# Kernel optimization log

Hardware: AMD Instinct MI355X
Metric: run time of the kernel (lower is better)

The kernel has to match this reference:

```python
import jax, jax.numpy as jnp
import numpy as np
from jax import lax

STEPS = 4
MULT = 4
N_MIX = 14  # sum(2+i for i in range(STEPS))
BN_SCALE = float(1.0 / np.sqrt(1.0 + 1e-5))  # eval-mode BatchNorm, affine=False, default running stats (mean=0, var=1)


def _bn(x):
    return x * jnp.asarray(BN_SCALE, x.dtype)


def _conv1x1(x, w):  # x [B,Ci,H,W], w [Co,Ci]
    return jnp.einsum('bihw,oi->bohw', x, w)


def _dwconv(x, w, pad, dil=1):  # depthwise conv, w [C,k,k]
    C = w.shape[0]
    return lax.conv_general_dilated(x, w[:, None], (1, 1),
                                    [(pad, pad), (pad, pad)],
                                    rhs_dilation=(dil, dil),
                                    dimension_numbers=('NCHW', 'OIHW', 'NCHW'),
                                    feature_group_count=C)


def _maxpool3(x):
    return lax.reduce_window(x, -jnp.inf, lax.max, (1, 1, 3, 3), (1, 1, 1, 1),
                             [(0, 0), (0, 0), (1, 1), (1, 1)])


def _avgpool3(x):  # count_include_pad=False as in torch avg_pool2d used by DARTS
    s = lax.reduce_window(x, 0.0, lax.add, (1, 1, 3, 3), (1, 1, 1, 1),
                          [(0, 0), (0, 0), (1, 1), (1, 1)])
    ones = jnp.ones(x.shape[2:], x.dtype)
    cnt = lax.reduce_window(ones, 0.0, lax.add, (3, 3), (1, 1), [(1, 1), (1, 1)])
    return s / cnt


def _sep_conv(x, dw1, pw1, dw2, pw2, pad):
    y = _bn(_conv1x1(_dwconv(jax.nn.relu(x), dw1, pad), pw1))
    return _bn(_conv1x1(_dwconv(jax.nn.relu(y), dw2, pad), pw2))


def _dil_conv(x, dw, pw, pad):
    return _bn(_conv1x1(_dwconv(jax.nn.relu(x), dw, pad, dil=2), pw))


def setup_inputs():
    key = jax.random.key(0)
    B, C_in, C, H, W = 32, 512, 128, 32, 32
    ks = jax.random.split(key, 24)
    rn = lambda k, shp, s=0.05: jax.random.normal(k, shp, jnp.float32) * s
    return {
        's0': jax.random.normal(ks[0], (B, C_in, H, W), jnp.float32),
        's1': jax.random.normal(ks[1], (B, C_in, H, W), jnp.float32),
        'gates': jax.random.normal(ks[2], (N_MIX, B, 8), jnp.float32),
        'pre0_w': rn(ks[3], (C, C_in)),
        'pre1_w': rn(ks[4], (C, C_in)),
        'sep3_dw1': rn(ks[5], (N_MIX, C, 3, 3), 0.2),
        'sep3_pw1': rn(ks[6], (N_MIX, C, C)),
        'sep3_dw2': rn(ks[7], (N_MIX, C, 3, 3), 0.2),
        'sep3_pw2': rn(ks[8], (N_MIX, C, C)),
        'sep5_dw1': rn(ks[9], (N_MIX, C, 5, 5), 0.2),
        'sep5_pw1': rn(ks[10], (N_MIX, C, C)),
        'sep5_dw2': rn(ks[11], (N_MIX, C, 5, 5), 0.2),
        'sep5_pw2': rn(ks[12], (N_MIX, C, C)),
        'dil3_dw': rn(ks[13], (N_MIX, C, 3, 3), 0.2),
        'dil3_pw': rn(ks[14], (N_MIX, C, C)),
        'dil5_dw': rn(ks[15], (N_MIX, C, 5, 5), 0.2),
        'dil5_pw': rn(ks[16], (N_MIX, C, C)),
        'top': 2,
    }


def reference(s0, s1, gates, pre0_w, pre1_w,
              sep3_dw1, sep3_pw1, sep3_dw2, sep3_pw2,
              sep5_dw1, sep5_pw1, sep5_dw2, sep5_pw2,
              dil3_dw, dil3_pw, dil5_dw, dil5_pw, top):
    def mixed(x, gate, m):
        # MixedOp.forward with external weights (is_first=False): top-k mask,
        # masked softmax -> per-sample alphas that are exactly 0 off the top-k,
        # weighted sum over candidate ops (dense form of the scatter-add dispatch).
        B = gate.shape[0]
        _, idx = lax.top_k(gate, top)  # [B, top]
        mask = jnp.zeros(gate.shape, bool).at[jnp.arange(B)[:, None], idx].set(True)
        p = jax.nn.softmax(jnp.where(mask, gate, -jnp.inf), axis=-1)  # [B, 8]
        w = lambda o: p[:, o][:, None, None, None]
        # PRIMITIVES order: none, max_pool_3x3, avg_pool_3x3, skip_connect,
        #                   sep_conv_3x3, sep_conv_5x5, dil_conv_3x3, dil_conv_5x5
        out = w(1) * _bn(_maxpool3(x)) + w(2) * _bn(_avgpool3(x)) + w(3) * x
        out = out + w(4) * _sep_conv(x, sep3_dw1[m], sep3_pw1[m], sep3_dw2[m], sep3_pw2[m], 1)
        out = out + w(5) * _sep_conv(x, sep5_dw1[m], sep5_pw1[m], sep5_dw2[m], sep5_pw2[m], 2)
        out = out + w(6) * _dil_conv(x, dil3_dw[m], dil3_pw[m], 2)
        out = out + w(7) * _dil_conv(x, dil5_dw[m], dil5_pw[m], 4)
        return out

    # preprocess0/1: ReLUConvBN 1x1 (reduction_prev=False)
    s0 = _bn(_conv1x1(jax.nn.relu(s0), pre0_w))
    s1 = _bn(_conv1x1(jax.nn.relu(s1), pre1_w))
    states = [s0, s1]
    offset = 0
    for i in range(STEPS):
        s = sum(mixed(h, gates[offset + j], offset + j) for j, h in enumerate(states))
        offset += len(states)
        states.append(s)
    return jnp.concatenate(states[-MULT:], axis=1)  # [B, MULT*C, H, W]
```

## Files before the change

### kernel.cpp

```cpp
#include <hip/hip_runtime.h>

#define BN_S 0.9999950000374997f

typedef __attribute__((ext_vector_type(8))) short bf16x8;
typedef __attribute__((ext_vector_type(4))) float f32x4;

__device__ inline short f2bf(float f) {
    union { float f; unsigned u; } v; v.f = f;
    return (short)((v.u + 0x7FFFu + ((v.u >> 16) & 1u)) >> 16);
}

__global__ void gates_k(const float* __restrict__ g, const int* __restrict__ topp,
                        float* __restrict__ p)
{
    int t = blockIdx.x * blockDim.x + threadIdx.x;
    if (t >= 14 * 32) return;
    int top = topp[0];
    float v[8]; bool sel[8];
    for (int o = 0; o < 8; ++o) { v[o] = g[t * 8 + o]; sel[o] = false; }
    for (int it = 0; it < top; ++it) {
        int bi = 0; float bv = -3.4e38f;
        for (int o = 0; o < 8; ++o)
            if (!sel[o] && v[o] > bv) { bv = v[o]; bi = o; }
        sel[bi] = true;
    }
    float mx = -3.4e38f;
    for (int o = 0; o < 8; ++o) if (sel[o]) mx = fmaxf(mx, v[o]);
    float e[8]; float sum = 0.0f;
    for (int o = 0; o < 8; ++o) { e[o] = sel[o] ? expf(v[o] - mx) : 0.0f; sum += e[o]; }
    for (int o = 0; o < 8; ++o) p[t * 8 + o] = e[o] / sum;
}

__global__ void cvt_k(const float* __restrict__ s3p1, const float* __restrict__ s3p2,
                      const float* __restrict__ s5p1, const float* __restrict__ s5p2,
                      const float* __restrict__ d3p,  const float* __restrict__ d5p,
                      const float* __restrict__ pre0, const float* __restrict__ pre1,
                      short* __restrict__ wb, short* __restrict__ wpre)
{
    const int which = blockIdx.y;
    const float* src; short* dst; int n;
    switch (which) {
        case 0: src = s3p1; dst = wb;               n = 229376; break;
        case 1: src = s3p2; dst = wb + 229376;      n = 229376; break;
        case 2: src = s5p1; dst = wb + 2 * 229376;  n = 229376; break;
        case 3: src = s5p2; dst = wb + 3 * 229376;  n = 229376; break;
        case 4: src = d3p;  dst = wb + 4 * 229376;  n = 229376; break;
        case 5: src = d5p;  dst = wb + 5 * 229376;  n = 229376; break;
        case 6: src = pre0; dst = wpre;             n = 65536;  break;
        default:src = pre1; dst = wpre + 65536;     n = 65536;  break;
    }
    for (int i = blockIdx.x * 256 + threadIdx.x; i < n; i += gridDim.x * 256)
        dst[i] = f2bf(src[i]);
}

__global__ void __launch_bounds__(256)
pre_k(const float* __restrict__ s0, const float* __restrict__ s1,
      const short* __restrict__ wpre,
      float* __restrict__ s0p, float* __restrict__ s1p)
{
    const int z = blockIdx.z;
    const int b = z & 31, which = z >> 5;
    const float* in = (which ? s1 : s0) + (long)b * 524288;
    const short* w = wpre + which * 65536;
    float* outp = (which ? s1p : s0p) + (long)b * 131072;

    const int tid = threadIdx.x;
    const int wave = tid >> 6, lane = tid & 63;
    const int quad = lane >> 4, l16 = lane & 15;
    const int n0 = blockIdx.x * 128;

    __shared__ short bt[128 * 40];
    const int tn = tid & 127, tk = (tid >> 7) * 16;

    f32x4 acc[16];
#pragma unroll
    for (int i = 0; i < 16; ++i) acc[i] = (f32x4){0.f, 0.f, 0.f, 0.f};

    for (int k0 = 0; k0 < 512; k0 += 32) {
        __syncthreads();
        bf16x8 lo, hi;
#pragma unroll
        for (int kk = 0; kk < 8; ++kk) {
            lo[kk] = f2bf(fmaxf(in[(long)(k0 + tk + kk) * 1024 + n0 + tn], 0.0f));
            hi[kk] = f2bf(fmaxf(in[(long)(k0 + tk + 8 + kk) * 1024 + n0 + tn], 0.0f));
        }
        *(bf16x8*)&bt[tn * 40 + tk]     = lo;
        *(bf16x8*)&bt[tn * 40 + tk + 8] = hi;
        __syncthreads();
#pragma unroll
        for (int cf = 0; cf < 2; ++cf) {
            bf16x8 af = *(const bf16x8*)(w + (long)(wave * 32 + cf * 16 + l16) * 512
                                           + k0 + quad * 8);
#pragma unroll
            for (int s = 0; s < 8; ++s) {
                bf16x8 bfv = *(const bf16x8*)&bt[(s * 16 + l16) * 40 + quad * 8];
                acc[cf * 8 + s] = __builtin_amdgcn_mfma_f32_16x16x32_bf16(
                                      af, bfv, acc[cf * 8 + s], 0, 0, 0);
            }
        }
    }
#pragma unroll
    for (int cf = 0; cf < 2; ++cf)
#pragma unroll
        for (int s = 0; s < 8; ++s)
#pragma unroll
            for (int r = 0; r < 4; ++r)
                outp[(long)(wave * 32 + cf * 16 + quad * 4 + r) * 1024
                     + n0 + s * 16 + l16] = acc[cf * 8 + s][r] * BN_S;
}

template<int KS, int DIL, int PAD>
__device__ inline float dwc(const float* t, const float* w, int h, int wx) {
    float s = 0.0f;
#pragma unroll
    for (int ki = 0; ki < KS; ++ki) {
        int y = h - PAD + ki * DIL;
        if ((unsigned)y < 32u) {
#pragma unroll
            for (int kj = 0; kj < KS; ++kj) {
                int x = wx - PAD + kj * DIL;
                if ((unsigned)x < 32u) s += w[ki * KS + kj] * t[(y << 5) + x];
            }
        }
    }
    return s;
}

struct BranchA {
    const float* xs[5]; long xbs[5];
    int goff[5]; int m[5]; int nb;
};


__global__ void __launch_bounds__(256)
dw1_all(BranchA a, const float* __restrict__ s3d1, const float* __restrict__ s5d1,
        const float* __restrict__ d3d, const float* __restrict__ d5d,
        short* __restrict__ X, const float* __restrict__ p)
{
    const int c = blockIdx.x, b = blockIdx.y, j = blockIdx.z;
    const float* pm = p + a.goff[j] + b * 8;
    const float g4 = pm[4], g5 = pm[5], g6 = pm[6], g7 = pm[7];
    if (g4 == 0.f && g5 == 0.f && g6 == 0.f && g7 == 0.f) return;
    const int m = a.m[j];
    __shared__ float t[1024];
    __shared__ float wl[4][25];
    const int tid = threadIdx.x;
    const float* src = a.xs[j] + (long)b * a.xbs[j] + (long)c * 1024;
    for (int i = tid; i < 1024; i += 256) t[i] = fmaxf(src[i], 0.0f);
    if (tid < 9)                      wl[0][tid]     = s3d1[(long)m * 1152 + (long)c * 9 + tid];
    else if (tid >= 64 && tid < 89)   wl[1][tid-64]  = s5d1[(long)m * 3200 + (long)c * 25 + tid - 64];
    else if (tid >= 128 && tid < 137) wl[2][tid-128] = d3d[(long)m * 1152 + (long)c * 9 + tid - 128];
    else if (tid >= 192 && tid < 217) wl[3][tid-192] = d5d[(long)m * 3200 + (long)c * 25 + tid - 192];
    __syncthreads();
    short* dst = X + (long)j * 16777216 + (long)b * 524288 + (long)c * 1024;
    const float s6 = g6 * BN_S, s7 = g7 * BN_S;
    for (int i = tid; i < 1024; i += 256) {
        int h = i >> 5, wx = i & 31;
        if (g4 != 0.f) dst[i]          = f2bf(dwc<3,1,1>(t, wl[0], h, wx));
        if (g5 != 0.f) dst[131072 + i] = f2bf(dwc<5,1,2>(t, wl[1], h, wx));
        if (g6 != 0.f) dst[262144 + i] = f2bf(s6 * dwc<3,2,2>(t, wl[2], h, wx));
        if (g7 != 0.f) dst[393216 + i] = f2bf(s7 * dwc<5,2,4>(t, wl[3], h, wx));
    }
}

__global__ void __launch_bounds__(256)
pw1_all(BranchA a, const short* __restrict__ X, const short* __restrict__ wb,
        float* __restrict__ yb, const float* __restrict__ p)
{
    const int z = blockIdx.z, b = z & 31, j = z >> 5;
    const int u = blockIdx.y >> 2, cot = blockIdx.y & 3;
    if (p[a.goff[j] + b * 8 + 4 + u] == 0.f) return;
    const int tid = threadIdx.x;
    const int wave = tid >> 6, lane = tid & 63;
    const int quad = lane >> 4, l16 = lane & 15;
    const int co0 = cot * 32 + (wave & 1) * 16;
    const int n0  = blockIdx.x * 128 + (wave >> 1) * 64;
    const short* w = wb + (u ? 2L * 229376 : 0L) + (long)a.m[j] * 16384;
    const short* xb = X + (long)j * 16777216 + (long)b * 524288 + (long)u * 131072;

    f32x4 acc[4] = {{0,0,0,0},{0,0,0,0},{0,0,0,0},{0,0,0,0}};
    for (int k0 = 0; k0 < 128; k0 += 32) {
        bf16x8 af = *(const bf16x8*)(w + (co0 + l16) * 128 + k0 + quad * 8);
        const short* xc = xb + (long)(k0 + quad * 8) * 1024 + n0 + l16;
#pragma unroll
        for (int s = 0; s < 4; ++s) {
            bf16x8 bfv;
#pragma unroll
            for (int jj = 0; jj < 8; ++jj) bfv[jj] = xc[jj * 1024 + s * 16];
            acc[s] = __builtin_amdgcn_mfma_f32_16x16x32_bf16(af, bfv, acc[s], 0, 0, 0);
        }
    }
    float* dst = yb + (long)j * 8388608 + ((long)b * 2 + u) * 131072;
#pragma unroll
    for (int s = 0; s < 4; ++s)
#pragma unroll
        for (int r = 0; r < 4; ++r)
            dst[(long)(co0 + quad * 4 + r) * 1024 + n0 + s * 16 + l16] =
                fmaxf(acc[s][r] * BN_S, 0.0f);
}

__global__ void __launch_bounds__(256)
dw2_all(BranchA a, const float* __restrict__ yb,
        const float* __restrict__ s3d2, const float* __restrict__ s5d2,
        short* __restrict__ X, const float* __restrict__ p)
{
    const int c = blockIdx.x, b = blockIdx.y;
    const int z = blockIdx.z, u = z & 1, j = z >> 1;
    const float g = p[a.goff[j] + b * 8 + 4 + u];
    if (g == 0.f) return;
    const int m = a.m[j];
    __shared__ float t[1024];
    __shared__ float wl[25];
    const int tid = threadIdx.x;
    const float* src = yb + (long)j * 8388608 + ((long)b * 2 + u) * 131072 + (long)c * 1024;
    for (int i = tid; i < 1024; i += 256) t[i] = src[i];
    if (u == 0) { if (tid < 9)  wl[tid] = s3d2[(long)m * 1152 + (long)c * 9  + tid]; }
    else        { if (tid < 25) wl[tid] = s5d2[(long)m * 3200 + (long)c * 25 + tid]; }
    __syncthreads();
    const float sc = g * BN_S;
    short* dst = X + (long)j * 16777216 + (long)b * 524288 + (long)u * 131072 + (long)c * 1024;
    if (u == 0) {
        for (int i = tid; i < 1024; i += 256)
            dst[i] = f2bf(sc * dwc<3,1,1>(t, wl, i >> 5, i & 31));
    } else {
        for (int i = tid; i < 1024; i += 256)
            dst[i] = f2bf(sc * dwc<5,1,2>(t, wl, i >> 5, i & 31));
    }
}

__global__ void __launch_bounds__(256)
final_all(BranchA a, const short* __restrict__ X, const short* __restrict__ wb,
          float* __restrict__ outp, const float* __restrict__ p)
{
    const int b = blockIdx.z;
    const int tid = threadIdx.x;
    const int wave = tid >> 6, lane = tid & 63;
    const int quad = lane >> 4, l16 = lane & 15;
    const int co0 = blockIdx.y * 32 + (wave & 1) * 16;
    const int n0  = blockIdx.x * 128 + (wave >> 1) * 64;

    f32x4 acc[4] = {{0,0,0,0},{0,0,0,0},{0,0,0,0},{0,0,0,0}};
    bool any = false;
    for (int j = 0; j < a.nb; ++j) {
        const float* pm = p + a.goff[j] + b * 8;
        const short* xj = X + (long)j * 16777216 + (long)b * 524288;
        const long wm = (long)a.m[j] * 16384;
        const short* ws_[4] = { wb + 1L * 229376 + wm, wb + 3L * 229376 + wm,
                                wb + 4L * 229376 + wm, wb + 5L * 229376 + wm };
#pragma unroll
        for (int seg = 0; seg < 4; ++seg) {
            if (pm[4 + seg] == 0.f) continue;
            any = true;
            const short* w = ws_[seg];
            const short* xs = xj + (long)seg * 131072;
            for (int k0 = 0; k0 < 128; k0 += 32) {
                bf16x8 af = *(const bf16x8*)(w + (co0 + l16) * 128 + k0 + quad * 8);
                const short* xc = xs + (long)(k0 + quad * 8) * 1024 + n0 + l16;
#pragma unroll
                for (int s = 0; s < 4; ++s) {
                    bf16x8 bfv;
#pragma unroll
                    for (int jj = 0; jj < 8; ++jj) bfv[jj] = xc[jj * 1024 + s * 16];
                    acc[s] = __builtin_amdgcn_mfma_f32_16x16x32_bf16(af, bfv, acc[s], 0, 0, 0);
                }
            }
        }
    }
    if (!any) return;
#pragma unroll
    for (int s = 0; s < 4; ++s)
#pragma unroll
        for (int r = 0; r < 4; ++r) {
            long idx = (long)b * 524288 + (long)(co0 + quad * 4 + r) * 1024
                     + n0 + s * 16 + l16;
            outp[idx] += acc[s][r];
        }
}

struct PoolA { const float* xs[5]; long xbs[5]; int goff[5]; int cnt; };

__global__ void __launch_bounds__(256)
pool_skip_all_k(PoolA a, const float* __restrict__ p,
                float* __restrict__ so, long out_bs)
{
    const int c = blockIdx.x, b = blockIdx.y, tid = threadIdx.x;
    __shared__ float t[1024];
    float acc[4] = {0.f, 0.f, 0.f, 0.f};
    for (int j = 0; j < a.cnt; ++j) {
        const float* g = p + a.goff[j] + b * 8;
        float w1 = g[1] * BN_S, w2 = g[2] * BN_S, w3 = g[3];
        if (w1 == 0.f && w2 == 0.f && w3 == 0.f) continue;
        const float* src = a.xs[j] + (long)b * a.xbs[j] + (long)c * 1024;
        __syncthreads();
        for (int i = tid; i < 1024; i += 256) t[i] = src[i];
        __syncthreads();
#pragma unroll
        for (int e = 0; e < 4; ++e) {
            int i = tid + e * 256;
            int h = i >> 5, wx = i & 31;
            int y0 = max(h - 1, 0), y1 = min(h + 1, 31);
            int x0 = max(wx - 1, 0), x1 = min(wx + 1, 31);
            float mx = -3.4e38f, sm = 0.0f;
            for (int y = y0; y <= y1; ++y)
                for (int x = x0; x <= x1; ++x) {
                    float v = t[(y << 5) + x];
                    mx = fmaxf(mx, v); sm += v;
                }
            float cntc = (float)((y1 - y0 + 1) * (x1 - x0 + 1));
            acc[e] += w1 * mx + w2 * (sm / cntc) + w3 * t[i];
        }
    }
    float* dst = so + (long)b * out_bs + (long)c * 1024;
#pragma unroll
    for (int e = 0; e < 4; ++e) dst[tid + e * 256] = acc[e];
}

extern "C" void kernel_launch(void* const* d_in, const int* in_sizes, int n_in,
                              void* d_out, int out_size, void* d_ws, size_t ws_size,
                              hipStream_t stream)
{
    const float* s0   = (const float*)d_in[0];
    const float* s1   = (const float*)d_in[1];
    const float* gts  = (const float*)d_in[2];
    const float* pre0 = (const float*)d_in[3];
    const float* pre1 = (const float*)d_in[4];
    const float* s3d1 = (const float*)d_in[5];
    const float* s3p1 = (const float*)d_in[6];
    const float* s3d2 = (const float*)d_in[7];
    const float* s3p2 = (const float*)d_in[8];
    const float* s5d1 = (const float*)d_in[9];
    const float* s5p1 = (const float*)d_in[10];
    const float* s5d2 = (const float*)d_in[11];
    const float* s5p2 = (const float*)d_in[12];
    const float* d3d  = (const float*)d_in[13];
    const float* d3p  = (const float*)d_in[14];
    const float* d5d  = (const float*)d_in[15];
    const float* d5p  = (const float*)d_in[16];
    const int*   topp = (const int*)d_in[17];
    float* out = (float*)d_out;

    float* ws   = (float*)d_ws;
    float* p    = ws;
    float* s0p  = ws + 4096;
    float* s1p  = s0p + 4194304;
    short* wb   = (short*)(s1p + 4194304);
    short* wpre = wb + 1376256;
    char*  sl   = (char*)(wpre + 131072);
    uintptr_t ua = ((uintptr_t)sl + 255) & ~(uintptr_t)255;
    short* X    = (short*)ua;

    size_t used_base = (size_t)((char*)ua - (char*)d_ws);
    const size_t slot_bytes = 16777216ull * 2 + 8388608ull * 4;
    int nslot = 1;
    if (ws_size > used_base + slot_bytes)
        nslot = (int)((ws_size - used_base) / slot_bytes);
    if (nslot > 5) nslot = 5;
    if (nslot < 1) nslot = 1;
    float* yb = (float*)(X + (long)nslot * 16777216);

    gates_k<<<2, 256, 0, stream>>>(gts, topp, p);
    cvt_k<<<dim3(224, 8), 256, 0, stream>>>(s3p1, s3p2, s5p1, s5p2, d3p, d5p,
                                            pre0, pre1, wb, wpre);
    pre_k<<<dim3(8, 1, 64), 256, 0, stream>>>(s0, s1, wpre, s0p, s1p);

    const long SB = 131072L, OB = 524288L;
    const float* stp[6]; long sbs[6];
    stp[0] = s0p; sbs[0] = SB;
    stp[1] = s1p; sbs[1] = SB;

    int offset = 0;
    for (int i = 0; i < 4; ++i) {
        float* so = out + (long)i * 131072;
        int cnt = 2 + i;

        PoolA pa{};
        for (int j = 0; j < cnt; ++j) {
            pa.xs[j] = stp[j]; pa.xbs[j] = sbs[j]; pa.goff[j] = (offset + j) * 256;
        }
        pa.cnt = cnt;
        pool_skip_all_k<<<dim3(128, 32), 256, 0, stream>>>(pa, p, so, OB);

        for (int j0 = 0; j0 < cnt; j0 += nslot) {
            int nb = (cnt - j0 < nslot) ? (cnt - j0) : nslot;
            BranchA a{};
            for (int jj = 0; jj < nb; ++jj) {
                int j = j0 + jj, m = offset + j;
                a.xs[jj] = stp[j]; a.xbs[jj] = sbs[j];
                a.goff[jj] = m * 256; a.m[jj] = m;
            }
            a.nb = nb;
            dw1_all<<<dim3(128, 32, nb), 256, 0, stream>>>(a, s3d1, s5d1, d3d, d5d, X, p);
            pw1_all<<<dim3(8, 8, 32 * nb), 256, 0, stream>>>(a, X, wb, yb, p);
            dw2_all<<<dim3(128, 32, 2 * nb), 256, 0, stream>>>(a, yb, s3d2, s5d2, X, p);
            final_all<<<dim3(8, 4, 32), 256, 0, stream>>>(a, X, wb, so, p);
        }
        stp[2 + i] = so; sbs[2 + i] = OB;
        offset += cnt;
    }
}
```

Measured before the change: 935.2 us.

## Pad depthwise tiles in LDS, compute 4 outputs per thread, widen pre_k

The depthwise conv kernels now stage a zero-padded halo tile in shared memory, which removes the per-tap bounds checks. Each thread computes four adjacent output pixels and writes them as a single packed 4x bf16 store, so neighbouring taps are reused from registers. The preprocess GEMM kernel moves to 512 threads per block, with each wave handling 16 output channels instead of 32. This raises wave count per tile and halves the accumulator registers per thread, at the cost of more threads sharing each shared-memory tile load.

```diff
diff --git a/kernel.cpp b/kernel.cpp
--- a/kernel.cpp
+++ b/kernel.cpp
@@ -3,6 +3,7 @@
 #define BN_S 0.9999950000374997f
 
 typedef __attribute__((ext_vector_type(8))) short bf16x8;
+typedef __attribute__((ext_vector_type(4))) short s16x4;
 typedef __attribute__((ext_vector_type(4))) float f32x4;
 
 __device__ inline short f2bf(float f) {
@@ -53,7 +54,7 @@
         dst[i] = f2bf(src[i]);
 }
 
-__global__ void __launch_bounds__(256)
+__global__ void __launch_bounds__(512)
 pre_k(const float* __restrict__ s0, const float* __restrict__ s1,
       const short* __restrict__ wpre,
       float* __restrict__ s0p, float* __restrict__ s1p)
@@ -70,60 +71,33 @@
     const int n0 = blockIdx.x * 128;
 
     __shared__ short bt[128 * 40];
-    const int tn = tid & 127, tk = (tid >> 7) * 16;
-
-    f32x4 acc[16];
-#pragma unroll
-    for (int i = 0; i < 16; ++i) acc[i] = (f32x4){0.f, 0.f, 0.f, 0.f};
+    const int tn = tid & 127, tk = (tid >> 7) * 8;
+
+    f32x4 acc[8];
+#pragma unroll
+    for (int i = 0; i < 8; ++i) acc[i] = (f32x4){0.f, 0.f, 0.f, 0.f};
 
     for (int k0 = 0; k0 < 512; k0 += 32) {
         __syncthreads();
-        bf16x8 lo, hi;
-#pragma unroll
-        for (int kk = 0; kk < 8; ++kk) {
-            lo[kk] = f2bf(fmaxf(in[(long)(k0 + tk + kk) * 1024 + n0 + tn], 0.0f));
-            hi[kk] = f2bf(fmaxf(in[(long)(k0 + tk + 8 + kk) * 1024 + n0 + tn], 0.0f));
-        }
-        *(bf16x8*)&bt[tn * 40 + tk]     = lo;
-        *(bf16x8*)&bt[tn * 40 + tk + 8] = hi;
+        bf16x8 v;
+#pragma unroll
+        for (int kk = 0; kk < 8; ++kk)
+            v[kk] = f2bf(fmaxf(in[(long)(k0 + tk + kk) * 1024 + n0 + tn], 0.0f));
+        *(bf16x8*)&bt[tn * 40 + tk] = v;
         __syncthreads();
-#pragma unroll
-        for (int cf = 0; cf < 2; ++cf) {
-            bf16x8 af = *(const bf16x8*)(w + (long)(wave * 32 + cf * 16 + l16) * 512
-                                           + k0 + quad * 8);
-#pragma unroll
-            for (int s = 0; s < 8; ++s) {
-                bf16x8 bfv = *(const bf16x8*)&bt[(s * 16 + l16) * 40 + quad * 8];
-                acc[cf * 8 + s] = __builtin_amdgcn_mfma_f32_16x16x32_bf16(
-                                      af, bfv, acc[cf * 8 + s], 0, 0, 0);
-            }
-        }
-    }
-#pragma unroll
-    for (int cf = 0; cf < 2; ++cf)
-#pragma unroll
-        for (int s = 0; s < 8; ++s)
-#pragma unroll
-            for (int r = 0; r < 4; ++r)
-                outp[(long)(wave * 32 + cf * 16 + quad * 4 + r) * 1024
-                     + n0 + s * 16 + l16] = acc[cf * 8 + s][r] * BN_S;
-}
-
-template<int KS, int DIL, int PAD>
-__device__ inline float dwc(const float* t, const float* w, int h, int wx) {
-    float s = 0.0f;
-#pragma unroll
-    for (int ki = 0; ki < KS; ++ki) {
-        int y = h - PAD + ki * DIL;
-        if ((unsigned)y < 32u) {
-#pragma unroll
-            for (int kj = 0; kj < KS; ++kj) {
-                int x = wx - PAD + kj * DIL;
-                if ((unsigned)x < 32u) s += w[ki * KS + kj] * t[(y << 5) + x];
-            }
-        }
-    }
-    return s;
+        bf16x8 af = *(const bf16x8*)(w + (long)(wave * 16 + l16) * 512 + k0 + quad * 8);
+#pragma unroll
+        for (int s = 0; s < 8; ++s) {
+            bf16x8 bfv = *(const bf16x8*)&bt[(s * 16 + l16) * 40 + quad * 8];
+            acc[s] = __builtin_amdgcn_mfma_f32_16x16x32_bf16(af, bfv, acc[s], 0, 0, 0);
+        }
+    }
+#pragma unroll
+    for (int s = 0; s < 8; ++s)
+#pragma unroll
+        for (int r = 0; r < 4; ++r)
+            outp[(long)(wave * 16 + quad * 4 + r) * 1024 + n0 + s * 16 + l16] =
+                acc[s][r] * BN_S;
 }
 
 struct BranchA {
@@ -142,24 +116,86 @@
     const float g4 = pm[4], g5 = pm[5], g6 = pm[6], g7 = pm[7];
     if (g4 == 0.f && g5 == 0.f && g6 == 0.f && g7 == 0.f) return;
     const int m = a.m[j];
-    __shared__ float t[1024];
+    __shared__ float t[40 * 40];
     __shared__ float wl[4][25];
     const int tid = threadIdx.x;
     const float* src = a.xs[j] + (long)b * a.xbs[j] + (long)c * 1024;
-    for (int i = tid; i < 1024; i += 256) t[i] = fmaxf(src[i], 0.0f);
+    for (int i = tid; i < 1600; i += 256) {
+        int r = i / 40, col = i - r * 40;
+        int y = r - 4, x = col - 4;
+        float v = 0.0f;
+        if ((unsigned)y < 32u && (unsigned)x < 32u) v = fmaxf(src[(y << 5) + x], 0.0f);
+        t[i] = v;
+    }
     if (tid < 9)                      wl[0][tid]     = s3d1[(long)m * 1152 + (long)c * 9 + tid];
     else if (tid >= 64 && tid < 89)   wl[1][tid-64]  = s5d1[(long)m * 3200 + (long)c * 25 + tid - 64];
     else if (tid >= 128 && tid < 137) wl[2][tid-128] = d3d[(long)m * 1152 + (long)c * 9 + tid - 128];
     else if (tid >= 192 && tid < 217) wl[3][tid-192] = d5d[(long)m * 3200 + (long)c * 25 + tid - 192];
     __syncthreads();
     short* dst = X + (long)j * 16777216 + (long)b * 524288 + (long)c * 1024;
+    const int h = tid >> 3, w0 = (tid & 7) * 4;
+    const float* tc = &t[(h + 4) * 40 + (w0 + 4)];
     const float s6 = g6 * BN_S, s7 = g7 * BN_S;
-    for (int i = tid; i < 1024; i += 256) {
-        int h = i >> 5, wx = i & 31;
-        if (g4 != 0.f) dst[i]          = f2bf(dwc<3,1,1>(t, wl[0], h, wx));
-        if (g5 != 0.f) dst[131072 + i] = f2bf(dwc<5,1,2>(t, wl[1], h, wx));
-        if (g6 != 0.f) dst[262144 + i] = f2bf(s6 * dwc<3,2,2>(t, wl[2], h, wx));
-        if (g7 != 0.f) dst[393216 + i] = f2bf(s7 * dwc<5,2,4>(t, wl[3], h, wx));
+
+    if (g4 != 0.f) {
+        float a0 = 0.f, a1 = 0.f, a2 = 0.f, a3 = 0.f;
+#pragma unroll
+        for (int ki = 0; ki < 3; ++ki) {
+            const float* row = tc + (ki - 1) * 40;
+#pragma unroll
+            for (int kj = 0; kj < 3; ++kj) {
+                float wv = wl[0][ki * 3 + kj];
+                a0 += wv * row[kj - 1]; a1 += wv * row[kj];
+                a2 += wv * row[kj + 1]; a3 += wv * row[kj + 2];
+            }
+        }
+        *(s16x4*)&dst[tid * 4] = (s16x4){f2bf(a0), f2bf(a1), f2bf(a2), f2bf(a3)};
+    }
+    if (g5 != 0.f) {
+        float a0 = 0.f, a1 = 0.f, a2 = 0.f, a3 = 0.f;
+#pragma unroll
+        for (int ki = 0; ki < 5; ++ki) {
+            const float* row = tc + (ki - 2) * 40;
+#pragma unroll
+            for (int kj = 0; kj < 5; ++kj) {
+                float wv = wl[1][ki * 5 + kj];
+                a0 += wv * row[kj - 2]; a1 += wv * row[kj - 1];
+                a2 += wv * row[kj];     a3 += wv * row[kj + 1];
+            }
+        }
+        *(s16x4*)&dst[131072 + tid * 4] = (s16x4){f2bf(a0), f2bf(a1), f2bf(a2), f2bf(a3)};
+    }
+    if (g6 != 0.f) {
+        float a0 = 0.f, a1 = 0.f, a2 = 0.f, a3 = 0.f;
+#pragma unroll
+        for (int ki = 0; ki < 3; ++ki) {
+            const float* row = tc + (ki * 2 - 2) * 40;
+#pragma unroll
+            for (int kj = 0; kj < 3; ++kj) {
+                float wv = wl[2][ki * 3 + kj];
+                int o = kj * 2 - 2;
+                a0 += wv * row[o];     a1 += wv * row[o + 1];
+                a2 += wv * row[o + 2]; a3 += wv * row[o + 3];
+            }
+        }
+        *(s16x4*)&dst[262144 + tid * 4] =
+            (s16x4){f2bf(s6 * a0), f2bf(s6 * a1), f2bf(s6 * a2), f2bf(s6 * a3)};
+    }
+    if (g7 != 0.f) {
+        float a0 = 0.f, a1 = 0.f, a2 = 0.f, a3 = 0.f;
+#pragma unroll
+        for (int ki = 0; ki < 5; ++ki) {
+            const float* row = tc + (ki * 2 - 4) * 40;
+#pragma unroll
+            for (int kj = 0; kj < 5; ++kj) {
+                float wv = wl[3][ki * 5 + kj];
+                int o = kj * 2 - 4;
+                a0 += wv * row[o];     a1 += wv * row[o + 1];
+                a2 += wv * row[o + 2]; a3 += wv * row[o + 3];
+            }
+        }
+        *(s16x4*)&dst[393216 + tid * 4] =
+            (s16x4){f2bf(s7 * a0), f2bf(s7 * a1), f2bf(s7 * a2), f2bf(s7 * a3)};
     }
 }
 
@@ -209,23 +245,50 @@
     const float g = p[a.goff[j] + b * 8 + 4 + u];
     if (g == 0.f) return;
     const int m = a.m[j];
-    __shared__ float t[1024];
+    __shared__ float t[36 * 36];
     __shared__ float wl[25];
     const int tid = threadIdx.x;
     const float* src = yb + (long)j * 8388608 + ((long)b * 2 + u) * 131072 + (long)c * 1024;
-    for (int i = tid; i < 1024; i += 256) t[i] = src[i];
+    for (int i = tid; i < 1296; i += 256) {
+        int r = i / 36, col = i - r * 36;
+        int y = r - 2, x = col - 2;
+        float v = 0.0f;
+        if ((unsigned)y < 32u && (unsigned)x < 32u) v = src[(y << 5) + x];
+        t[i] = v;
+    }
     if (u == 0) { if (tid < 9)  wl[tid] = s3d2[(long)m * 1152 + (long)c * 9  + tid]; }
     else        { if (tid < 25) wl[tid] = s5d2[(long)m * 3200 + (long)c * 25 + tid]; }
     __syncthreads();
     const float sc = g * BN_S;
     short* dst = X + (long)j * 16777216 + (long)b * 524288 + (long)u * 131072 + (long)c * 1024;
+    const int h = tid >> 3, w0 = (tid & 7) * 4;
+    const float* tc = &t[(h + 2) * 36 + (w0 + 2)];
+    float a0 = 0.f, a1 = 0.f, a2 = 0.f, a3 = 0.f;
     if (u == 0) {
-        for (int i = tid; i < 1024; i += 256)
-            dst[i] = f2bf(sc * dwc<3,1,1>(t, wl, i >> 5, i & 31));
+#pragma unroll
+        for (int ki = 0; ki < 3; ++ki) {
+            const float* row = tc + (ki - 1) * 36;
+#pragma unroll
+            for (int kj = 0; kj < 3; ++kj) {
+                float wv = wl[ki * 3 + kj];
+                a0 += wv * row[kj - 1]; a1 += wv * row[kj];
+                a2 += wv * row[kj + 1]; a3 += wv * row[kj + 2];
+            }
+        }
     } else {
-        for (int i = tid; i < 1024; i += 256)
-            dst[i] = f2bf(sc * dwc<5,1,2>(t, wl, i >> 5, i & 31));
-    }
+#pragma unroll
+        for (int ki = 0; ki < 5; ++ki) {
+            const float* row = tc + (ki - 2) * 36;
+#pragma unroll
+            for (int kj = 0; kj < 5; ++kj) {
+                float wv = wl[ki * 5 + kj];
+                a0 += wv * row[kj - 2]; a1 += wv * row[kj - 1];
+                a2 += wv * row[kj];     a3 += wv * row[kj + 1];
+            }
+        }
+    }
+    *(s16x4*)&dst[tid * 4] =
+        (s16x4){f2bf(sc * a0), f2bf(sc * a1), f2bf(sc * a2), f2bf(sc * a3)};
 }
 
 __global__ void __launch_bounds__(256)
@@ -361,7 +424,7 @@
     gates_k<<<2, 256, 0, stream>>>(gts, topp, p);
     cvt_k<<<dim3(224, 8), 256, 0, stream>>>(s3p1, s3p2, s5p1, s5p2, d3p, d5p,
                                             pre0, pre1, wb, wpre);
-    pre_k<<<dim3(8, 1, 64), 256, 0, stream>>>(s0, s1, wpre, s0p, s1p);
+    pre_k<<<dim3(8, 1, 64), 512, 0, stream>>>(s0, s1, wpre, s0p, s1p);
 
     const long SB = 131072L, OB = 524288L;
     const float* stp[6]; long sbs[6];
```

Result: faster. 814.7 us (-12.9%).

## Store depthwise outputs channel-interleaved and register-prefetch preprocess GEMM

Applied to the files above, without the earlier changes.

The depthwise kernels now process groups of 8 channels per block from a zero-padded shared tile. They write bf16 outputs in a [channel-group][pixel][8] interleaved layout, so the pointwise MFMA kernels can load each B fragment with one 16-byte vector load instead of eight strided scalar loads. The preprocess GEMM is retiled to 64 columns with 512 threads and prefetches the next K slice into registers to overlap global loads with MFMA. The cost is more shared memory per depthwise block (about 51KB) and fewer depthwise blocks, which may reduce occupancy.

```diff
diff --git a/kernel.cpp b/kernel.cpp
--- a/kernel.cpp
+++ b/kernel.cpp
@@ -3,6 +3,7 @@
 #define BN_S 0.9999950000374997f
 
 typedef __attribute__((ext_vector_type(8))) short bf16x8;
+typedef __attribute__((ext_vector_type(4))) short s16x4;
 typedef __attribute__((ext_vector_type(4))) float f32x4;
 
 __device__ inline short f2bf(float f) {
@@ -53,7 +54,7 @@
         dst[i] = f2bf(src[i]);
 }
 
-__global__ void __launch_bounds__(256)
+__global__ void __launch_bounds__(512)
 pre_k(const float* __restrict__ s0, const float* __restrict__ s1,
       const short* __restrict__ wpre,
       float* __restrict__ s0p, float* __restrict__ s1p)
@@ -67,63 +68,45 @@
     const int tid = threadIdx.x;
     const int wave = tid >> 6, lane = tid & 63;
     const int quad = lane >> 4, l16 = lane & 15;
-    const int n0 = blockIdx.x * 128;
-
-    __shared__ short bt[128 * 40];
-    const int tn = tid & 127, tk = (tid >> 7) * 16;
-
-    f32x4 acc[16];
-#pragma unroll
-    for (int i = 0; i < 16; ++i) acc[i] = (f32x4){0.f, 0.f, 0.f, 0.f};
+    const int n0 = blockIdx.x * 64;
+
+    __shared__ short bt[64 * 40];
+    const int tn = tid & 63, tk4 = (tid >> 6) * 4;
+
+    float r[4];
+#pragma unroll
+    for (int kk = 0; kk < 4; ++kk)
+        r[kk] = in[(long)(tk4 + kk) * 1024 + n0 + tn];
+
+    f32x4 acc[4];
+#pragma unroll
+    for (int i = 0; i < 4; ++i) acc[i] = (f32x4){0.f, 0.f, 0.f, 0.f};
 
     for (int k0 = 0; k0 < 512; k0 += 32) {
         __syncthreads();
-        bf16x8 lo, hi;
-#pragma unroll
-        for (int kk = 0; kk < 8; ++kk) {
-            lo[kk] = f2bf(fmaxf(in[(long)(k0 + tk + kk) * 1024 + n0 + tn], 0.0f));
-            hi[kk] = f2bf(fmaxf(in[(long)(k0 + tk + 8 + kk) * 1024 + n0 + tn], 0.0f));
-        }
-        *(bf16x8*)&bt[tn * 40 + tk]     = lo;
-        *(bf16x8*)&bt[tn * 40 + tk + 8] = hi;
+        s16x4 v;
+#pragma unroll
+        for (int kk = 0; kk < 4; ++kk) v[kk] = f2bf(fmaxf(r[kk], 0.0f));
+        *(s16x4*)&bt[tn * 40 + tk4] = v;
         __syncthreads();
-#pragma unroll
-        for (int cf = 0; cf < 2; ++cf) {
-            bf16x8 af = *(const bf16x8*)(w + (long)(wave * 32 + cf * 16 + l16) * 512
-                                           + k0 + quad * 8);
-#pragma unroll
-            for (int s = 0; s < 8; ++s) {
-                bf16x8 bfv = *(const bf16x8*)&bt[(s * 16 + l16) * 40 + quad * 8];
-                acc[cf * 8 + s] = __builtin_amdgcn_mfma_f32_16x16x32_bf16(
-                                      af, bfv, acc[cf * 8 + s], 0, 0, 0);
-            }
-        }
-    }
-#pragma unroll
-    for (int cf = 0; cf < 2; ++cf)
-#pragma unroll
-        for (int s = 0; s < 8; ++s)
-#pragma unroll
-            for (int r = 0; r < 4; ++r)
-                outp[(long)(wave * 32 + cf * 16 + quad * 4 + r) * 1024
-                     + n0 + s * 16 + l16] = acc[cf * 8 + s][r] * BN_S;
-}
-
-template<int KS, int DIL, int PAD>
-__device__ inline float dwc(const float* t, const float* w, int h, int wx) {
-    float s = 0.0f;
-#pragma unroll
-    for (int ki = 0; ki < KS; ++ki) {
-        int y = h - PAD + ki * DIL;
-        if ((unsigned)y < 32u) {
-#pragma unroll
-            for (int kj = 0; kj < KS; ++kj) {
-                int x = wx - PAD + kj * DIL;
-                if ((unsigned)x < 32u) s += w[ki * KS + kj] * t[(y << 5) + x];
-            }
-        }
-    }
-    return s;
+        if (k0 < 480) {
+#pragma unroll
+            for (int kk = 0; kk < 4; ++kk)
+                r[kk] = in[(long)(k0 + 32 + tk4 + kk) * 1024 + n0 + tn];
+        }
+        bf16x8 af = *(const bf16x8*)(w + (long)(wave * 16 + l16) * 512 + k0 + quad * 8);
+#pragma unroll
+        for (int s = 0; s < 4; ++s) {
+            bf16x8 bfv = *(const bf16x8*)&bt[(s * 16 + l16) * 40 + quad * 8];
+            acc[s] = __builtin_amdgcn_mfma_f32_16x16x32_bf16(af, bfv, acc[s], 0, 0, 0);
+        }
+    }
+#pragma unroll
+    for (int s = 0; s < 4; ++s)
+#pragma unroll
+        for (int rr = 0; rr < 4; ++rr)
+            outp[(long)(wave * 16 + quad * 4 + rr) * 1024 + n0 + s * 16 + l16] =
+                acc[s][rr] * BN_S;
 }
 
 struct BranchA {
@@ -137,29 +120,100 @@
         const float* __restrict__ d3d, const float* __restrict__ d5d,
         short* __restrict__ X, const float* __restrict__ p)
 {
-    const int c = blockIdx.x, b = blockIdx.y, j = blockIdx.z;
+    const int cg = blockIdx.x, b = blockIdx.y, j = blockIdx.z;
     const float* pm = p + a.goff[j] + b * 8;
     const float g4 = pm[4], g5 = pm[5], g6 = pm[6], g7 = pm[7];
     if (g4 == 0.f && g5 == 0.f && g6 == 0.f && g7 == 0.f) return;
     const int m = a.m[j];
-    __shared__ float t[1024];
-    __shared__ float wl[4][25];
+    __shared__ float t[8][1600];
+    __shared__ float wl[4][8][25];
     const int tid = threadIdx.x;
-    const float* src = a.xs[j] + (long)b * a.xbs[j] + (long)c * 1024;
-    for (int i = tid; i < 1024; i += 256) t[i] = fmaxf(src[i], 0.0f);
-    if (tid < 9)                      wl[0][tid]     = s3d1[(long)m * 1152 + (long)c * 9 + tid];
-    else if (tid >= 64 && tid < 89)   wl[1][tid-64]  = s5d1[(long)m * 3200 + (long)c * 25 + tid - 64];
-    else if (tid >= 128 && tid < 137) wl[2][tid-128] = d3d[(long)m * 1152 + (long)c * 9 + tid - 128];
-    else if (tid >= 192 && tid < 217) wl[3][tid-192] = d5d[(long)m * 3200 + (long)c * 25 + tid - 192];
+    const int c0 = cg * 8;
+    const float* src = a.xs[j] + (long)b * a.xbs[j] + (long)c0 * 1024;
+    for (int i = tid; i < 8 * 1600; i += 256) {
+        int e = i / 1600, rr = i - e * 1600;
+        int row = rr / 40, col = rr - row * 40;
+        int y = row - 4, x = col - 4;
+        float v = 0.0f;
+        if ((unsigned)y < 32u && (unsigned)x < 32u)
+            v = fmaxf(src[e * 1024 + (y << 5) + x], 0.0f);
+        t[e][rr] = v;
+    }
+    for (int i = tid; i < 72; i += 256)
+        wl[0][i / 9][i % 9] = s3d1[(long)m * 1152 + (long)(c0 + i / 9) * 9 + i % 9];
+    for (int i = tid; i < 200; i += 256)
+        wl[1][i / 25][i % 25] = s5d1[(long)m * 3200 + (long)(c0 + i / 25) * 25 + i % 25];
+    for (int i = tid; i < 72; i += 256)
+        wl[2][i / 9][i % 9] = d3d[(long)m * 1152 + (long)(c0 + i / 9) * 9 + i % 9];
+    for (int i = tid; i < 200; i += 256)
+        wl[3][i / 25][i % 25] = d5d[(long)m * 3200 + (long)(c0 + i / 25) * 25 + i % 25];
     __syncthreads();
-    short* dst = X + (long)j * 16777216 + (long)b * 524288 + (long)c * 1024;
+    short* dst = X + (long)j * 16777216 + (long)b * 524288 + (long)cg * 8192;
     const float s6 = g6 * BN_S, s7 = g7 * BN_S;
-    for (int i = tid; i < 1024; i += 256) {
-        int h = i >> 5, wx = i & 31;
-        if (g4 != 0.f) dst[i]          = f2bf(dwc<3,1,1>(t, wl[0], h, wx));
-        if (g5 != 0.f) dst[131072 + i] = f2bf(dwc<5,1,2>(t, wl[1], h, wx));
-        if (g6 != 0.f) dst[262144 + i] = f2bf(s6 * dwc<3,2,2>(t, wl[2], h, wx));
-        if (g7 != 0.f) dst[393216 + i] = f2bf(s7 * dwc<5,2,4>(t, wl[3], h, wx));
+    for (int i = 0; i < 4; ++i) {
+        const int px = i * 256 + tid;
+        const int h = px >> 5, wx = px & 31;
+        const int base = (h + 4) * 40 + (wx + 4);
+        if (g4 != 0.f) {
+            bf16x8 o;
+#pragma unroll
+            for (int e = 0; e < 8; ++e) {
+                const float* te = &t[e][base];
+                float s = 0.f;
+#pragma unroll
+                for (int ki = 0; ki < 3; ++ki)
+#pragma unroll
+                    for (int kj = 0; kj < 3; ++kj)
+                        s += wl[0][e][ki * 3 + kj] * te[(ki - 1) * 40 + (kj - 1)];
+                o[e] = f2bf(s);
+            }
+            *(bf16x8*)&dst[px * 8] = o;
+        }
+        if (g5 != 0.f) {
+            bf16x8 o;
+#pragma unroll
+            for (int e = 0; e < 8; ++e) {
+                const float* te = &t[e][base];
+                float s = 0.f;
+#pragma unroll
+                for (int ki = 0; ki < 5; ++ki)
+#pragma unroll
+                    for (int kj = 0; kj < 5; ++kj)
+                        s += wl[1][e][ki * 5 + kj] * te[(ki - 2) * 40 + (kj - 2)];
+                o[e] = f2bf(s);
+            }
+            *(bf16x8*)&dst[131072 + px * 8] = o;
+        }
+        if (g6 != 0.f) {
+            bf16x8 o;
+#pragma unroll
+            for (int e = 0; e < 8; ++e) {
+                const float* te = &t[e][base];
+                float s = 0.f;
+#pragma unroll
+                for (int ki = 0; ki < 3; ++ki)
+#pragma unroll
+                    for (int kj = 0; kj < 3; ++kj)
+                        s += wl[2][e][ki * 3 + kj] * te[(ki * 2 - 2) * 40 + (kj * 2 - 2)];
+                o[e] = f2bf(s6 * s);
+            }
+            *(bf16x8*)&dst[262144 + px * 8] = o;
+        }
+        if (g7 != 0.f) {
+            bf16x8 o;
+#pragma unroll
+            for (int e = 0; e < 8; ++e) {
+                const float* te = &t[e][base];
+                float s = 0.f;
+#pragma unroll
+                for (int ki = 0; ki < 5; ++ki)
+#pragma unroll
+                    for (int kj = 0; kj < 5; ++kj)
+                        s += wl[3][e][ki * 5 + kj] * te[(ki * 2 - 4) * 40 + (kj * 2 - 4)];
+                o[e] = f2bf(s7 * s);
+            }
+            *(bf16x8*)&dst[393216 + px * 8] = o;
+        }
     }
 }
 
@@ -181,12 +235,10 @@
     f32x4 acc[4] = {{0,0,0,0},{0,0,0,0},{0,0,0,0},{0,0,0,0}};
     for (int k0 = 0; k0 < 128; k0 += 32) {
         bf16x8 af = *(const bf16x8*)(w + (co0 + l16) * 128 + k0 + quad * 8);
-        const short* xc = xb + (long)(k0 + quad * 8) * 1024 + n0 + l16;
+        const short* xg = xb + (long)((k0 >> 3) + quad) * 8192;
 #pragma unroll
         for (int s = 0; s < 4; ++s) {
-            bf16x8 bfv;
-#pragma unroll
-            for (int jj = 0; jj < 8; ++jj) bfv[jj] = xc[jj * 1024 + s * 16];
+            bf16x8 bfv = *(const bf16x8*)&xg[(n0 + s * 16 + l16) * 8];
             acc[s] = __builtin_amdgcn_mfma_f32_16x16x32_bf16(af, bfv, acc[s], 0, 0, 0);
         }
     }
@@ -204,27 +256,67 @@
         const float* __restrict__ s3d2, const float* __restrict__ s5d2,
         short* __restrict__ X, const float* __restrict__ p)
 {
-    const int c = blockIdx.x, b = blockIdx.y;
+    const int cg = blockIdx.x, b = blockIdx.y;
     const int z = blockIdx.z, u = z & 1, j = z >> 1;
     const float g = p[a.goff[j] + b * 8 + 4 + u];
     if (g == 0.f) return;
     const int m = a.m[j];
-    __shared__ float t[1024];
-    __shared__ float wl[25];
+    __shared__ float t[8][1296];
+    __shared__ float wl[8][25];
     const int tid = threadIdx.x;
-    const float* src = yb + (long)j * 8388608 + ((long)b * 2 + u) * 131072 + (long)c * 1024;
-    for (int i = tid; i < 1024; i += 256) t[i] = src[i];
-    if (u == 0) { if (tid < 9)  wl[tid] = s3d2[(long)m * 1152 + (long)c * 9  + tid]; }
-    else        { if (tid < 25) wl[tid] = s5d2[(long)m * 3200 + (long)c * 25 + tid]; }
+    const int c0 = cg * 8;
+    const float* src = yb + (long)j * 8388608 + ((long)b * 2 + u) * 131072
+                     + (long)c0 * 1024;
+    for (int i = tid; i < 8 * 1296; i += 256) {
+        int e = i / 1296, rr = i - e * 1296;
+        int row = rr / 36, col = rr - row * 36;
+        int y = row - 2, x = col - 2;
+        float v = 0.0f;
+        if ((unsigned)y < 32u && (unsigned)x < 32u) v = src[e * 1024 + (y << 5) + x];
+        t[e][rr] = v;
+    }
+    if (u == 0) {
+        for (int i = tid; i < 72; i += 256)
+            wl[i / 9][i % 9] = s3d2[(long)m * 1152 + (long)(c0 + i / 9) * 9 + i % 9];
+    } else {
+        for (int i = tid; i < 200; i += 256)
+            wl[i / 25][i % 25] = s5d2[(long)m * 3200 + (long)(c0 + i / 25) * 25 + i % 25];
+    }
     __syncthreads();
     const float sc = g * BN_S;
-    short* dst = X + (long)j * 16777216 + (long)b * 524288 + (long)u * 131072 + (long)c * 1024;
-    if (u == 0) {
-        for (int i = tid; i < 1024; i += 256)
-            dst[i] = f2bf(sc * dwc<3,1,1>(t, wl, i >> 5, i & 31));
-    } else {
-        for (int i = tid; i < 1024; i += 256)
-            dst[i] = f2bf(sc * dwc<5,1,2>(t, wl, i >> 5, i & 31));
+    short* dst = X + (long)j * 16777216 + (long)b * 524288 + (long)u * 131072
+               + (long)cg * 8192;
+    for (int i = 0; i < 4; ++i) {
+        const int px = i * 256 + tid;
+        const int h = px >> 5, wx = px & 31;
+        const int base = (h + 2) * 36 + (wx + 2);
+        bf16x8 o;
+        if (u == 0) {
+#pragma unroll
+            for (int e = 0; e < 8; ++e) {
+                const float* te = &t[e][base];
+                float s = 0.f;
+#pragma unroll
+                for (int ki = 0; ki < 3; ++ki)
+#pragma unroll
+                    for (int kj = 0; kj < 3; ++kj)
+                        s += wl[e][ki * 3 + kj] * te[(ki - 1) * 36 + (kj - 1)];
+                o[e] = f2bf(sc * s);
+            }
+        } else {
+#pragma unroll
+            for (int e = 0; e < 8; ++e) {
+                const float* te = &t[e][base];
+                float s = 0.f;
+#pragma unroll
+                for (int ki = 0; ki < 5; ++ki)
+#pragma unroll
+                    for (int kj = 0; kj < 5; ++kj)
+                        s += wl[e][ki * 5 + kj] * te[(ki - 2) * 36 + (kj - 2)];
+                o[e] = f2bf(sc * s);
+            }
+        }
+        *(bf16x8*)&dst[px * 8] = o;
     }
 }
 
@@ -255,12 +347,10 @@
             const short* xs = xj + (long)seg * 131072;
             for (int k0 = 0; k0 < 128; k0 += 32) {
                 bf16x8 af = *(const bf16x8*)(w + (co0 + l16) * 128 + k0 + quad * 8);
-                const short* xc = xs + (long)(k0 + quad * 8) * 1024 + n0 + l16;
+                const short* xg = xs + (long)((k0 >> 3) + quad) * 8192;
 #pragma unroll
                 for (int s = 0; s < 4; ++s) {
-                    bf16x8 bfv;
-#pragma unroll
-                    for (int jj = 0; jj < 8; ++jj) bfv[jj] = xc[jj * 1024 + s * 16];
+                    bf16x8 bfv = *(const bf16x8*)&xg[(n0 + s * 16 + l16) * 8];
                     acc[s] = __builtin_amdgcn_mfma_f32_16x16x32_bf16(af, bfv, acc[s], 0, 0, 0);
                 }
             }
@@ -361,7 +451,7 @@
     gates_k<<<2, 256, 0, stream>>>(gts, topp, p);
     cvt_k<<<dim3(224, 8), 256, 0, stream>>>(s3p1, s3p2, s5p1, s5p2, d3p, d5p,
                                             pre0, pre1, wb, wpre);
-    pre_k<<<dim3(8, 1, 64), 256, 0, stream>>>(s0, s1, wpre, s0p, s1p);
+    pre_k<<<dim3(16, 1, 64), 512, 0, stream>>>(s0, s1, wpre, s0p, s1p);
 
     const long SB = 131072L, OB = 524288L;
     const float* stp[6]; long sbs[6];
@@ -389,9 +479,9 @@
                 a.goff[jj] = m * 256; a.m[jj] = m;
             }
             a.nb = nb;
-            dw1_all<<<dim3(128, 32, nb), 256, 0, stream>>>(a, s3d1, s5d1, d3d, d5d, X, p);
+            dw1_all<<<dim3(16, 32, nb), 256, 0, stream>>>(a, s3d1, s5d1, d3d, d5d, X, p);
             pw1_all<<<dim3(8, 8, 32 * nb), 256, 0, stream>>>(a, X, wb, yb, p);
-            dw2_all<<<dim3(128, 32, 2 * nb), 256, 0, stream>>>(a, yb, s3d2, s5d2, X, p);
+            dw2_all<<<dim3(16, 32, 2 * nb), 256, 0, stream>>>(a, yb, s3d2, s5d2, X, p);
             final_all<<<dim3(8, 4, 32), 256, 0, stream>>>(a, X, wb, so, p);
         }
         stp[2 + i] = so; sbs[2 + i] = OB;
```

After: 1.506 ms. 1.61x slower.
